# Kernel optimization log

Measured on AMD Instinct MI355X. Metric: run time of the kernel, lower is better.

Reference implementation:

```python
import jax, jax.numpy as jnp
import numpy as np

B, C, N = 4, 256, 4096
OUT = 256
TEMP = OUT ** 0.5  # temperature = sqrt(out_channel)


def setup_inputs() -> dict:
    key = jax.random.key(0)
    kx, kxx, kq, kk, kv = jax.random.split(key, 5)
    x = jax.random.normal(kx, (B, C, N), dtype=jnp.float32)
    xx = jax.random.normal(kxx, (B, C, N), dtype=jnp.float32)
    # Conv1d(in, out, kernel=1, bias=False) weights, squeezed to (out, in)
    s = 1.0 / np.sqrt(C)
    Wq = jax.random.uniform(kq, (OUT, C), jnp.float32, -s, s)
    Wk = jax.random.uniform(kk, (OUT, C), jnp.float32, -s, s)
    Wv = jax.random.uniform(kv, (OUT, C), jnp.float32, -s, s)
    return {"x": x, "xx": xx, "Wq": Wq, "Wk": Wk, "Wv": Wv}


def reference(x, xx, Wq, Wk, Wv):
    # 1x1 conv == per-point linear: (out,in) x (b,in,n) -> (b,out,n)
    q = jnp.einsum('oc,bcn->bon', Wq, x)
    k = jnp.einsum('oc,bcn->bon', Wk, xx)
    v = jnp.einsum('oc,bcn->bon', Wv, xx)
    # attn = (q^T / temp) @ k : (B, N, N)
    attn = jax.nn.softmax(jnp.einsum('bon,bom->bnm', q, k) / TEMP, axis=-1)
    # dropout is identity in eval mode
    # y = attn @ v^T -> (B, N, OUT); returned transposed to (B, OUT, N)
    y = jnp.einsum('bnm,bom->bon', attn, v)
    return y
```

## Files before the change

### kernel.cpp

```cpp
#include <hip/hip_runtime.h>
#include <hip/hip_bf16.h>


typedef __attribute__((ext_vector_type(8))) short bf16x8;
typedef __attribute__((ext_vector_type(4))) float f32x4;
typedef __attribute__((ext_vector_type(4))) short short4t;

constexpr int B_ = 4;
constexpr int C_ = 256;
constexpr int N_ = 4096;
constexpr int O_ = 256;
constexpr float INV_TEMP = 1.0f / 16.0f;
constexpr int NIT = 64;

__device__ __forceinline__ short f2bf(float f) {
  union { float f; unsigned u; } v; v.f = f;
  unsigned r = v.u + 0x7fffu + ((v.u >> 16) & 1u);
  return (short)(r >> 16);
}

__device__ __forceinline__ void dma16(const short* g, short* l) {
  __builtin_amdgcn_global_load_lds(
      (const __attribute__((address_space(1))) unsigned int*)g,
      (__attribute__((address_space(3))) unsigned int*)l, 16, 0, 0);
}

__global__ void wcvt(const float* __restrict__ Wq, const float* __restrict__ Wk,
                     const float* __restrict__ Wv, short* __restrict__ wb) {
  int i = blockIdx.x * 256 + threadIdx.x;
  int mat = i >> 16, off = i & 65535;
  const float* W = (mat == 0) ? Wq : (mat == 1 ? Wk : Wv);
  wb[i] = f2bf(W[off]);
}

__global__ __launch_bounds__(256, 2) void qkv_proj(
    const float* __restrict__ x, const float* __restrict__ xx,
    const short* __restrict__ wb,
    short* __restrict__ qg, short* __restrict__ kt, short* __restrict__ vt) {
  const int n0  = blockIdx.x * 64;
  const int b   = blockIdx.y;
  const int mat = blockIdx.z;
  const float* src = (mat == 0) ? x : xx;
  const short* W   = wb + mat * 65536;
  const int tid = threadIdx.x;
  const int w = tid >> 6, lane = tid & 63;
  const int g = lane >> 4, c16 = lane & 15;

  __shared__ __align__(16) short xs[64][264];

  {
    const int n = tid & 63, cq = tid >> 6;
    const float* sp = src + (size_t)b * C_ * N_ + n0 + n;
#pragma unroll
    for (int rep = 0; rep < 16; ++rep) {
      int c = rep * 16 + cq * 4;
      short4t s4;
#pragma unroll
      for (int j = 0; j < 4; ++j) s4[j] = f2bf(sp[(size_t)(c + j) * N_]);
      *(short4t*)&xs[n][c] = s4;
    }
  }
  __syncthreads();

  f32x4 acc[4][4];
#pragma unroll
  for (int i = 0; i < 4; ++i)
#pragma unroll
    for (int j = 0; j < 4; ++j) acc[i][j] = (f32x4){0.f, 0.f, 0.f, 0.f};

#pragma unroll
  for (int ko = 0; ko < 8; ++ko) {
    bf16x8 wfr[4], xfr[4];
#pragma unroll
    for (int ot = 0; ot < 4; ++ot)
      wfr[ot] = *(const bf16x8*)&W[(w * 64 + ot * 16 + c16) * C_ + ko * 32 + g * 8];
#pragma unroll
    for (int nt = 0; nt < 4; ++nt)
      xfr[nt] = *(const bf16x8*)&xs[nt * 16 + c16][ko * 32 + g * 8];
    if (mat < 2) {
#pragma unroll
      for (int ot = 0; ot < 4; ++ot)
#pragma unroll
        for (int nt = 0; nt < 4; ++nt)
          acc[ot][nt] = __builtin_amdgcn_mfma_f32_16x16x32_bf16(
              wfr[ot], xfr[nt], acc[ot][nt], 0, 0, 0);
    } else {
#pragma unroll
      for (int mt = 0; mt < 4; ++mt)
#pragma unroll
        for (int ot = 0; ot < 4; ++ot)
          acc[mt][ot] = __builtin_amdgcn_mfma_f32_16x16x32_bf16(
              xfr[mt], wfr[ot], acc[mt][ot], 0, 0, 0);
    }
  }

  __syncthreads();
  short* ob = &xs[0][0];

  if (mat == 0) {
#pragma unroll
    for (int ot = 0; ot < 4; ++ot)
#pragma unroll
      for (int nt = 0; nt < 4; ++nt) {
        int f = (nt * 16 + c16) * 256 + w * 64 + ot * 16 + g * 4;
        short4t s;
        s[0] = f2bf(acc[ot][nt][0] * INV_TEMP);
        s[1] = f2bf(acc[ot][nt][1] * INV_TEMP);
        s[2] = f2bf(acc[ot][nt][2] * INV_TEMP);
        s[3] = f2bf(acc[ot][nt][3] * INV_TEMP);
        *(short4t*)&ob[f] = s;
      }
  } else if (mat == 1) {
#pragma unroll
    for (int ot = 0; ot < 4; ++ot)
#pragma unroll
      for (int nt = 0; nt < 4; ++nt) {
        int koo = w * 2 + (ot >> 1);
        int pos = (((ot & 1) * 2 + (g >> 1)) ^ ((c16 >> 1) & 3));
        int f = nt * 4096 + koo * 512 + c16 * 32 + pos * 8 + (g & 1) * 4;
        short4t s;
        s[0] = f2bf(acc[ot][nt][0]);
        s[1] = f2bf(acc[ot][nt][1]);
        s[2] = f2bf(acc[ot][nt][2]);
        s[3] = f2bf(acc[ot][nt][3]);
        *(short4t*)&ob[f] = s;
      }
  } else {
#pragma unroll
    for (int mt = 0; mt < 4; ++mt)
#pragma unroll
      for (int ot = 0; ot < 4; ++ot) {
        int o = w * 64 + ot * 16 + c16;
        int pos = (mt * 2 + (g >> 1)) ^ (o & 7);
        int f = o * 64 + pos * 8 + (g & 1) * 4;
        short4t s;
        s[0] = f2bf(acc[mt][ot][0]);
        s[1] = f2bf(acc[mt][ot][1]);
        s[2] = f2bf(acc[mt][ot][2]);
        s[3] = f2bf(acc[mt][ot][3]);
        *(short4t*)&ob[f] = s;
      }
  }
  __syncthreads();

  short* dst = (mat == 0) ? qg + ((size_t)b * N_ + n0) * O_
             : (mat == 1) ? kt + (size_t)(b * 256 + (n0 >> 4)) * 4096
                          : vt + (size_t)(b * 64 + (n0 >> 6)) * 16384;
  const uint4* s4 = (const uint4*)ob;
  uint4* d4 = (uint4*)dst;
#pragma unroll
  for (int j = 0; j < 8; ++j) d4[j * 256 + tid] = s4[j * 256 + tid];
}

__global__ __launch_bounds__(512, 2) void flash_attn(
    const short* __restrict__ qg, const short* __restrict__ kt,
    const short* __restrict__ vt, float* __restrict__ out) {
  const int xg = blockIdx.x;
  const int b  = xg >> 1;
  const int n0 = (((xg & 1) << 5) + blockIdx.y) * 64;
  const int tid = threadIdx.x;
  const int w = tid >> 6, lane = tid & 63;
  const int g = lane >> 4, c16 = lane & 15;
  const bool prod = (w < 4);
  const int pw = w & 3;

  __shared__ short kb[2][16384];
  __shared__ short vb[2][16384];
  __shared__ short ps[2][64][72];
  __shared__ float lsum[4][64];

  const short* ktb = kt + (size_t)b * N_ * O_;
  const short* vtb = vt + (size_t)b * N_ * O_;

  bf16x8 qf[4][8];
  float lrun[4] = {0.f, 0.f, 0.f, 0.f};
  f32x4 oacc[4][4];
#pragma unroll
  for (int i = 0; i < 4; ++i)
#pragma unroll
    for (int j = 0; j < 4; ++j) oacc[i][j] = (f32x4){0.f, 0.f, 0.f, 0.f};

  if (prod) {
#pragma unroll
    for (int nt = 0; nt < 4; ++nt) {
      const short* qrow =
          qg + (size_t)(b * N_ + n0 + nt * 16 + c16) * O_ + g * 8;
#pragma unroll
      for (int ko = 0; ko < 8; ++ko)
        qf[nt][ko] = *(const bf16x8*)(qrow + ko * 32);
    }
    const short* src = ktb + (size_t)pw * 4096;
#pragma unroll
    for (int j = 0; j < 8; ++j)
      dma16(src + j * 512 + lane * 8, &kb[0][pw * 4096 + j * 512]);
  }
  __syncthreads();

  const int sw = (g ^ ((c16 >> 1) & 3)) * 8;

  for (int i = 0; i <= NIT; ++i) {
    if (prod) {
      if (i < NIT) {
        if (i + 1 < NIT) {
          const short* src = ktb + (size_t)(4 * (i + 1) + pw) * 4096;
          short* dst = &kb[(i + 1) & 1][pw * 4096];
#pragma unroll
          for (int j = 0; j < 8; ++j)
            dma16(src + j * 512 + lane * 8, dst + j * 512);
        }
        const short* ksl = &kb[i & 1][pw * 4096];
        f32x4 sacc[4];
#pragma unroll
        for (int nt = 0; nt < 4; ++nt) sacc[nt] = (f32x4){0.f, 0.f, 0.f, 0.f};
#pragma unroll
        for (int ko = 0; ko < 8; ++ko) {
          bf16x8 kf = *(const bf16x8*)&ksl[(ko * 16 + c16) * 32 + sw];
#pragma unroll
          for (int nt = 0; nt < 4; ++nt)
            sacc[nt] = __builtin_amdgcn_mfma_f32_16x16x32_bf16(
                kf, qf[nt][ko], sacc[nt], 0, 0, 0);
        }
#pragma unroll
        for (int nt = 0; nt < 4; ++nt) {
          short4t pb;
          float rs = 0.f;
#pragma unroll
          for (int r = 0; r < 4; ++r) {
            float p = __expf(sacc[nt][r]);
            rs += p;
            pb[r] = f2bf(p);
          }
          lrun[nt] += rs;
          *(short4t*)&ps[i & 1][nt * 16 + c16][pw * 16 + g * 4] = pb;
        }
      }
    } else {
      if (i < NIT) {
        const short* src = vtb + (size_t)i * 16384 + pw * 4096;
        short* dst = &vb[i & 1][pw * 4096];
#pragma unroll
        for (int j = 0; j < 8; ++j)
          dma16(src + j * 512 + lane * 8, dst + j * 512);
      }
      if (i > 0) {
        const int pb_ = (i - 1) & 1;
#pragma unroll
        for (int kk = 0; kk < 2; ++kk) {
          bf16x8 pf[4];
#pragma unroll
          for (int nt = 0; nt < 4; ++nt)
            pf[nt] = *(const bf16x8*)&ps[pb_][nt * 16 + c16][kk * 32 + g * 8];
#pragma unroll
          for (int ot = 0; ot < 4; ++ot) {
            int pos = (kk * 4 + g) ^ (c16 & 7);
            bf16x8 vf = *(const bf16x8*)
                &vb[pb_][(pw * 64 + ot * 16 + c16) * 64 + pos * 8];
#pragma unroll
            for (int nt = 0; nt < 4; ++nt)
              oacc[ot][nt] = __builtin_amdgcn_mfma_f32_16x16x32_bf16(
                  vf, pf[nt], oacc[ot][nt], 0, 0, 0);
          }
        }
      }
    }
    __syncthreads();
  }

  if (prod) {
#pragma unroll
    for (int nt = 0; nt < 4; ++nt) {
      float v = lrun[nt];
      v += __shfl_xor(v, 16);
      v += __shfl_xor(v, 32);
      if (lane < 16) lsum[pw][nt * 16 + lane] = v;
    }
  }
  __syncthreads();
  if (!prod) {
#pragma unroll
    for (int nt = 0; nt < 4; ++nt) {
      const int nl = nt * 16 + c16;
      float l = lsum[0][nl] + lsum[1][nl] + lsum[2][nl] + lsum[3][nl];
      float li = 1.0f / l;
#pragma unroll
      for (int ot = 0; ot < 4; ++ot) {
        float* op = out + ((size_t)b * O_ + pw * 64 + ot * 16 + g * 4) * N_ +
                    n0 + nl;
#pragma unroll
        for (int r = 0; r < 4; ++r)
          op[(size_t)r * N_] = oacc[ot][nt][r] * li;
      }
    }
  }
}

extern "C" void kernel_launch(void* const* d_in, const int* in_sizes, int n_in,
                              void* d_out, int out_size, void* d_ws,
                              size_t ws_size, hipStream_t stream) {
  const float* x  = (const float*)d_in[0];
  const float* xx = (const float*)d_in[1];
  const float* Wq = (const float*)d_in[2];
  const float* Wk = (const float*)d_in[3];
  const float* Wv = (const float*)d_in[4];
  float* out = (float*)d_out;

  short* qg = (short*)d_ws;
  short* kt = qg + (size_t)B_ * N_ * O_;
  short* vt = kt + (size_t)B_ * N_ * O_;
  short* wb = vt + (size_t)B_ * N_ * O_;

  wcvt<<<768, 256, 0, stream>>>(Wq, Wk, Wv, wb);
  qkv_proj<<<dim3(N_ / 64, B_, 3), 256, 0, stream>>>(x, xx, wb, qg, kt, vt);
  flash_attn<<<dim3(8, 32), 512, 0, stream>>>(qg, kt, vt, out);
}
```

Baseline: 207.3 us.

## Pre-transpose inputs to bf16 in a separate kernel and fold temperature into Wq

Adds an xpose kernel that DMAs fp32 x/xx tiles into LDS and writes them transposed as bf16 (N-major). It stages this scratch copy in the output buffer, which flash_attn later overwrites. qkv_proj then reads its MFMA operand fragments straight from global bf16 instead of doing strided fp32 loads and conversion into LDS. The 1/temperature scale moves into the Wq bf16 conversion, so the Q epilogue no longer multiplies. The cost is an extra launch and an extra write and read of the transposed inputs.

After: 217.0 us. 4.7% more time.

```diff
diff --git a/kernel.cpp b/kernel.cpp
--- a/kernel.cpp
+++ b/kernel.cpp
@@ -19,7 +19,7 @@
   return (short)(r >> 16);
 }
 
-__device__ __forceinline__ void dma16(const short* g, short* l) {
+__device__ __forceinline__ void dma16(const void* g, void* l) {
   __builtin_amdgcn_global_load_lds(
       (const __attribute__((address_space(1))) unsigned int*)g,
       (__attribute__((address_space(3))) unsigned int*)l, 16, 0, 0);
@@ -30,37 +30,58 @@
   int i = blockIdx.x * 256 + threadIdx.x;
   int mat = i >> 16, off = i & 65535;
   const float* W = (mat == 0) ? Wq : (mat == 1 ? Wk : Wv);
-  wb[i] = f2bf(W[off]);
+  float v = W[off];
+  if (mat == 0) v *= INV_TEMP;
+  wb[i] = f2bf(v);
+}
+
+__global__ __launch_bounds__(256, 2) void xpose(
+    const float* __restrict__ x, const float* __restrict__ xx,
+    short* __restrict__ xb) {
+  const int nt = blockIdx.x;
+  const int ct = blockIdx.y;
+  const int b  = blockIdx.z >> 1;
+  const int inp = blockIdx.z & 1;
+  const float* src = (inp ? xx : x) + (size_t)b * C_ * N_;
+  const int tid = threadIdx.x;
+  const int w = tid >> 6, lane = tid & 63;
+
+  __shared__ float tl[64][256];
+
+  {
+    const float* rp = src + (size_t)(ct * 64 + w * 16) * N_ + nt * 256 + lane * 4;
+#pragma unroll
+    for (int j = 0; j < 16; ++j)
+      dma16(rp + (size_t)j * N_, &tl[w * 16 + j][0]);
+  }
+  __syncthreads();
+
+  {
+    const int n = tid;
+    short* orow = xb + ((size_t)(inp * B_ + b) * N_ + nt * 256 + n) * C_ + ct * 64;
+#pragma unroll
+    for (int oct = 0; oct < 8; ++oct) {
+      bf16x8 v;
+#pragma unroll
+      for (int j = 0; j < 8; ++j) v[j] = f2bf(tl[oct * 8 + j][n]);
+      *(bf16x8*)(orow + oct * 8) = v;
+    }
+  }
 }
 
 __global__ __launch_bounds__(256, 2) void qkv_proj(
-    const float* __restrict__ x, const float* __restrict__ xx,
-    const short* __restrict__ wb,
+    const short* __restrict__ xb, const short* __restrict__ wb,
     short* __restrict__ qg, short* __restrict__ kt, short* __restrict__ vt) {
   const int n0  = blockIdx.x * 64;
   const int b   = blockIdx.y;
   const int mat = blockIdx.z;
-  const float* src = (mat == 0) ? x : xx;
+  const short* xbb = xb + (size_t)(((mat > 0) ? B_ : 0) + b) * N_ * C_;
   const short* W   = wb + mat * 65536;
   const int tid = threadIdx.x;
   const int w = tid >> 6, lane = tid & 63;
   const int g = lane >> 4, c16 = lane & 15;
 
-  __shared__ __align__(16) short xs[64][264];
-
-  {
-    const int n = tid & 63, cq = tid >> 6;
-    const float* sp = src + (size_t)b * C_ * N_ + n0 + n;
-#pragma unroll
-    for (int rep = 0; rep < 16; ++rep) {
-      int c = rep * 16 + cq * 4;
-      short4t s4;
-#pragma unroll
-      for (int j = 0; j < 4; ++j) s4[j] = f2bf(sp[(size_t)(c + j) * N_]);
-      *(short4t*)&xs[n][c] = s4;
-    }
-  }
-  __syncthreads();
+  __shared__ __align__(16) short obuf[16384];
 
   f32x4 acc[4][4];
 #pragma unroll
@@ -76,7 +97,8 @@
       wfr[ot] = *(const bf16x8*)&W[(w * 64 + ot * 16 + c16) * C_ + ko * 32 + g * 8];
 #pragma unroll
     for (int nt = 0; nt < 4; ++nt)
-      xfr[nt] = *(const bf16x8*)&xs[nt * 16 + c16][ko * 32 + g * 8];
+      xfr[nt] = *(const bf16x8*)
+          &xbb[(size_t)(n0 + nt * 16 + c16) * C_ + ko * 32 + g * 8];
     if (mat < 2) {
 #pragma unroll
       for (int ot = 0; ot < 4; ++ot)
@@ -94,9 +116,6 @@
     }
   }
 
-  __syncthreads();
-  short* ob = &xs[0][0];
-
   if (mat == 0) {
 #pragma unroll
     for (int ot = 0; ot < 4; ++ot)
@@ -104,11 +123,11 @@
       for (int nt = 0; nt < 4; ++nt) {
         int f = (nt * 16 + c16) * 256 + w * 64 + ot * 16 + g * 4;
         short4t s;
-        s[0] = f2bf(acc[ot][nt][0] * INV_TEMP);
-        s[1] = f2bf(acc[ot][nt][1] * INV_TEMP);
-        s[2] = f2bf(acc[ot][nt][2] * INV_TEMP);
-        s[3] = f2bf(acc[ot][nt][3] * INV_TEMP);
-        *(short4t*)&ob[f] = s;
+        s[0] = f2bf(acc[ot][nt][0]);
+        s[1] = f2bf(acc[ot][nt][1]);
+        s[2] = f2bf(acc[ot][nt][2]);
+        s[3] = f2bf(acc[ot][nt][3]);
+        *(short4t*)&obuf[f] = s;
       }
   } else if (mat == 1) {
 #pragma unroll
@@ -123,7 +142,7 @@
         s[1] = f2bf(acc[ot][nt][1]);
         s[2] = f2bf(acc[ot][nt][2]);
         s[3] = f2bf(acc[ot][nt][3]);
-        *(short4t*)&ob[f] = s;
+        *(short4t*)&obuf[f] = s;
       }
   } else {
 #pragma unroll
@@ -138,7 +157,7 @@
         s[1] = f2bf(acc[mt][ot][1]);
         s[2] = f2bf(acc[mt][ot][2]);
         s[3] = f2bf(acc[mt][ot][3]);
-        *(short4t*)&ob[f] = s;
+        *(short4t*)&obuf[f] = s;
       }
   }
   __syncthreads();
@@ -146,7 +165,7 @@
   short* dst = (mat == 0) ? qg + ((size_t)b * N_ + n0) * O_
              : (mat == 1) ? kt + (size_t)(b * 256 + (n0 >> 4)) * 4096
                           : vt + (size_t)(b * 64 + (n0 >> 6)) * 16384;
-  const uint4* s4 = (const uint4*)ob;
+  const uint4* s4 = (const uint4*)obuf;
   uint4* d4 = (uint4*)dst;
 #pragma unroll
   for (int j = 0; j < 8; ++j) d4[j * 256 + tid] = s4[j * 256 + tid];
@@ -303,6 +322,7 @@
   const float* Wk = (const float*)d_in[3];
   const float* Wv = (const float*)d_in[4];
   float* out = (float*)d_out;
+  short* xb = (short*)d_out;
 
   short* qg = (short*)d_ws;
   short* kt = qg + (size_t)B_ * N_ * O_;
@@ -310,6 +330,7 @@
   short* wb = vt + (size_t)B_ * N_ * O_;
 
   wcvt<<<768, 256, 0, stream>>>(Wq, Wk, Wv, wb);
-  qkv_proj<<<dim3(N_ / 64, B_, 3), 256, 0, stream>>>(x, xx, wb, qg, kt, vt);
+  xpose<<<dim3(16, 4, 8), 256, 0, stream>>>(x, xx, xb);
+  qkv_proj<<<dim3(N_ / 64, B_, 3), 256, 0, stream>>>(xb, wb, qg, kt, vt);
   flash_attn<<<dim3(8, 32), 512, 0, stream>>>(qg, kt, vt, out);
 }
```

## Double flash-attention waves per block and fold weight conversion into projection

Applied to the files above, without the earlier changes.

The flash attention block grows from 512 to 1024 threads. There are now 8 producer waves, each computing scores for half the query rows of a key slice, and 8 consumer waves, each owning 32 output channels instead of 64. This halves per-wave register state and MFMA work and aims to hide latency better with more waves per CU. The separate weight-conversion kernel is removed: qkv_proj now reads the fp32 weights directly, converts them to bf16 in-register and folds the 1/temp scale into Wq. That saves one launch, but every projection block repeats the weight conversion, and the launch-bounds hint of 4 blocks of 1024 threads may push register limits.

Result: slower. 229.4 us (+10.7%).

```diff
diff --git a/kernel.cpp b/kernel.cpp
--- a/kernel.cpp
+++ b/kernel.cpp
@@ -19,29 +19,23 @@
   return (short)(r >> 16);
 }
 
-__device__ __forceinline__ void dma16(const short* g, short* l) {
+__device__ __forceinline__ void dma16(const void* g, void* l) {
   __builtin_amdgcn_global_load_lds(
       (const __attribute__((address_space(1))) unsigned int*)g,
       (__attribute__((address_space(3))) unsigned int*)l, 16, 0, 0);
 }
 
-__global__ void wcvt(const float* __restrict__ Wq, const float* __restrict__ Wk,
-                     const float* __restrict__ Wv, short* __restrict__ wb) {
-  int i = blockIdx.x * 256 + threadIdx.x;
-  int mat = i >> 16, off = i & 65535;
-  const float* W = (mat == 0) ? Wq : (mat == 1 ? Wk : Wv);
-  wb[i] = f2bf(W[off]);
-}
-
 __global__ __launch_bounds__(256, 2) void qkv_proj(
     const float* __restrict__ x, const float* __restrict__ xx,
-    const short* __restrict__ wb,
+    const float* __restrict__ Wq, const float* __restrict__ Wk,
+    const float* __restrict__ Wv,
     short* __restrict__ qg, short* __restrict__ kt, short* __restrict__ vt) {
   const int n0  = blockIdx.x * 64;
   const int b   = blockIdx.y;
   const int mat = blockIdx.z;
   const float* src = (mat == 0) ? x : xx;
-  const short* W   = wb + mat * 65536;
+  const float* Wm  = (mat == 0) ? Wq : (mat == 1 ? Wk : Wv);
+  const float ws   = (mat == 0) ? INV_TEMP : 1.0f;
   const int tid = threadIdx.x;
   const int w = tid >> 6, lane = tid & 63;
   const int g = lane >> 4, c16 = lane & 15;
@@ -72,8 +66,18 @@
   for (int ko = 0; ko < 8; ++ko) {
     bf16x8 wfr[4], xfr[4];
 #pragma unroll
-    for (int ot = 0; ot < 4; ++ot)
-      wfr[ot] = *(const bf16x8*)&W[(w * 64 + ot * 16 + c16) * C_ + ko * 32 + g * 8];
+    for (int ot = 0; ot < 4; ++ot) {
+      const float* wp =
+          Wm + (size_t)(w * 64 + ot * 16 + c16) * C_ + ko * 32 + g * 8;
+      float4 f0 = *(const float4*)wp;
+      float4 f1 = *(const float4*)(wp + 4);
+      bf16x8 a;
+      a[0] = f2bf(f0.x * ws); a[1] = f2bf(f0.y * ws);
+      a[2] = f2bf(f0.z * ws); a[3] = f2bf(f0.w * ws);
+      a[4] = f2bf(f1.x * ws); a[5] = f2bf(f1.y * ws);
+      a[6] = f2bf(f1.z * ws); a[7] = f2bf(f1.w * ws);
+      wfr[ot] = a;
+    }
 #pragma unroll
     for (int nt = 0; nt < 4; ++nt)
       xfr[nt] = *(const bf16x8*)&xs[nt * 16 + c16][ko * 32 + g * 8];
@@ -104,10 +108,10 @@
       for (int nt = 0; nt < 4; ++nt) {
         int f = (nt * 16 + c16) * 256 + w * 64 + ot * 16 + g * 4;
         short4t s;
-        s[0] = f2bf(acc[ot][nt][0] * INV_TEMP);
-        s[1] = f2bf(acc[ot][nt][1] * INV_TEMP);
-        s[2] = f2bf(acc[ot][nt][2] * INV_TEMP);
-        s[3] = f2bf(acc[ot][nt][3] * INV_TEMP);
+        s[0] = f2bf(acc[ot][nt][0]);
+        s[1] = f2bf(acc[ot][nt][1]);
+        s[2] = f2bf(acc[ot][nt][2]);
+        s[3] = f2bf(acc[ot][nt][3]);
         *(short4t*)&ob[f] = s;
       }
   } else if (mat == 1) {
@@ -152,7 +156,7 @@
   for (int j = 0; j < 8; ++j) d4[j * 256 + tid] = s4[j * 256 + tid];
 }
 
-__global__ __launch_bounds__(512, 2) void flash_attn(
+__global__ __launch_bounds__(1024, 4) void flash_attn(
     const short* __restrict__ qg, const short* __restrict__ kt,
     const short* __restrict__ vt, float* __restrict__ out) {
   const int xg = blockIdx.x;
@@ -161,8 +165,10 @@
   const int tid = threadIdx.x;
   const int w = tid >> 6, lane = tid & 63;
   const int g = lane >> 4, c16 = lane & 15;
-  const bool prod = (w < 4);
-  const int pw = w & 3;
+  const bool prod = (w < 8);
+  const int ga = w & 3;
+  const int h  = (w >> 2) & 1;
+  const int cw = w & 7;
 
   __shared__ short kb[2][16384];
   __shared__ short vb[2][16384];
@@ -172,27 +178,28 @@
   const short* ktb = kt + (size_t)b * N_ * O_;
   const short* vtb = vt + (size_t)b * N_ * O_;
 
-  bf16x8 qf[4][8];
-  float lrun[4] = {0.f, 0.f, 0.f, 0.f};
-  f32x4 oacc[4][4];
-#pragma unroll
-  for (int i = 0; i < 4; ++i)
+  bf16x8 qf[2][8];
+  float lrun[2] = {0.f, 0.f};
+  f32x4 oacc[2][4];
+#pragma unroll
+  for (int i = 0; i < 2; ++i)
 #pragma unroll
     for (int j = 0; j < 4; ++j) oacc[i][j] = (f32x4){0.f, 0.f, 0.f, 0.f};
 
   if (prod) {
 #pragma unroll
-    for (int nt = 0; nt < 4; ++nt) {
+    for (int j = 0; j < 2; ++j) {
       const short* qrow =
-          qg + (size_t)(b * N_ + n0 + nt * 16 + c16) * O_ + g * 8;
+          qg + (size_t)(b * N_ + n0 + (h * 2 + j) * 16 + c16) * O_ + g * 8;
 #pragma unroll
       for (int ko = 0; ko < 8; ++ko)
-        qf[nt][ko] = *(const bf16x8*)(qrow + ko * 32);
-    }
-    const short* src = ktb + (size_t)pw * 4096;
-#pragma unroll
-    for (int j = 0; j < 8; ++j)
-      dma16(src + j * 512 + lane * 8, &kb[0][pw * 4096 + j * 512]);
+        qf[j][ko] = *(const bf16x8*)(qrow + ko * 32);
+    }
+    const short* src = ktb + (size_t)(w >> 1) * 4096 + (w & 1) * 2048;
+    short* dst = &kb[0][(w >> 1) * 4096 + (w & 1) * 2048];
+#pragma unroll
+    for (int j = 0; j < 4; ++j)
+      dma16(src + j * 512 + lane * 8, dst + j * 512);
   }
   __syncthreads();
 
@@ -202,44 +209,45 @@
     if (prod) {
       if (i < NIT) {
         if (i + 1 < NIT) {
-          const short* src = ktb + (size_t)(4 * (i + 1) + pw) * 4096;
-          short* dst = &kb[(i + 1) & 1][pw * 4096];
-#pragma unroll
-          for (int j = 0; j < 8; ++j)
+          const short* src =
+              ktb + (size_t)(4 * (i + 1) + (w >> 1)) * 4096 + (w & 1) * 2048;
+          short* dst = &kb[(i + 1) & 1][(w >> 1) * 4096 + (w & 1) * 2048];
+#pragma unroll
+          for (int j = 0; j < 4; ++j)
             dma16(src + j * 512 + lane * 8, dst + j * 512);
         }
-        const short* ksl = &kb[i & 1][pw * 4096];
-        f32x4 sacc[4];
-#pragma unroll
-        for (int nt = 0; nt < 4; ++nt) sacc[nt] = (f32x4){0.f, 0.f, 0.f, 0.f};
+        const short* ksl = &kb[i & 1][ga * 4096];
+        f32x4 sacc[2];
+        sacc[0] = (f32x4){0.f, 0.f, 0.f, 0.f};
+        sacc[1] = (f32x4){0.f, 0.f, 0.f, 0.f};
 #pragma unroll
         for (int ko = 0; ko < 8; ++ko) {
           bf16x8 kf = *(const bf16x8*)&ksl[(ko * 16 + c16) * 32 + sw];
 #pragma unroll
-          for (int nt = 0; nt < 4; ++nt)
-            sacc[nt] = __builtin_amdgcn_mfma_f32_16x16x32_bf16(
-                kf, qf[nt][ko], sacc[nt], 0, 0, 0);
+          for (int j = 0; j < 2; ++j)
+            sacc[j] = __builtin_amdgcn_mfma_f32_16x16x32_bf16(
+                kf, qf[j][ko], sacc[j], 0, 0, 0);
         }
 #pragma unroll
-        for (int nt = 0; nt < 4; ++nt) {
+        for (int j = 0; j < 2; ++j) {
           short4t pb;
           float rs = 0.f;
 #pragma unroll
           for (int r = 0; r < 4; ++r) {
-            float p = __expf(sacc[nt][r]);
+            float p = __expf(sacc[j][r]);
             rs += p;
             pb[r] = f2bf(p);
           }
-          lrun[nt] += rs;
-          *(short4t*)&ps[i & 1][nt * 16 + c16][pw * 16 + g * 4] = pb;
+          lrun[j] += rs;
+          *(short4t*)&ps[i & 1][(h * 2 + j) * 16 + c16][ga * 16 + g * 4] = pb;
         }
       }
     } else {
       if (i < NIT) {
-        const short* src = vtb + (size_t)i * 16384 + pw * 4096;
-        short* dst = &vb[i & 1][pw * 4096];
-#pragma unroll
-        for (int j = 0; j < 8; ++j)
+        const short* src = vtb + (size_t)i * 16384 + cw * 2048;
+        short* dst = &vb[i & 1][cw * 2048];
+#pragma unroll
+        for (int j = 0; j < 4; ++j)
           dma16(src + j * 512 + lane * 8, dst + j * 512);
       }
       if (i > 0) {
@@ -251,10 +259,10 @@
           for (int nt = 0; nt < 4; ++nt)
             pf[nt] = *(const bf16x8*)&ps[pb_][nt * 16 + c16][kk * 32 + g * 8];
 #pragma unroll
-          for (int ot = 0; ot < 4; ++ot) {
-            int pos = (kk * 4 + g) ^ (c16 & 7);
-            bf16x8 vf = *(const bf16x8*)
-                &vb[pb_][(pw * 64 + ot * 16 + c16) * 64 + pos * 8];
+          for (int ot = 0; ot < 2; ++ot) {
+            int o = cw * 32 + ot * 16 + c16;
+            int pos = (kk * 4 + g) ^ (o & 7);
+            bf16x8 vf = *(const bf16x8*)&vb[pb_][o * 64 + pos * 8];
 #pragma unroll
             for (int nt = 0; nt < 4; ++nt)
               oacc[ot][nt] = __builtin_amdgcn_mfma_f32_16x16x32_bf16(
@@ -268,11 +276,11 @@
 
   if (prod) {
 #pragma unroll
-    for (int nt = 0; nt < 4; ++nt) {
-      float v = lrun[nt];
+    for (int j = 0; j < 2; ++j) {
+      float v = lrun[j];
       v += __shfl_xor(v, 16);
       v += __shfl_xor(v, 32);
-      if (lane < 16) lsum[pw][nt * 16 + lane] = v;
+      if (lane < 16) lsum[ga][h * 32 + j * 16 + lane] = v;
     }
   }
   __syncthreads();
@@ -283,8 +291,8 @@
       float l = lsum[0][nl] + lsum[1][nl] + lsum[2][nl] + lsum[3][nl];
       float li = 1.0f / l;
 #pragma unroll
-      for (int ot = 0; ot < 4; ++ot) {
-        float* op = out + ((size_t)b * O_ + pw * 64 + ot * 16 + g * 4) * N_ +
+      for (int ot = 0; ot < 2; ++ot) {
+        float* op = out + ((size_t)b * O_ + cw * 32 + ot * 16 + g * 4) * N_ +
                     n0 + nl;
 #pragma unroll
         for (int r = 0; r < 4; ++r)
@@ -307,9 +315,8 @@
   short* qg = (short*)d_ws;
   short* kt = qg + (size_t)B_ * N_ * O_;
   short* vt = kt + (size_t)B_ * N_ * O_;
-  short* wb = vt + (size_t)B_ * N_ * O_;
-
-  wcvt<<<768, 256, 0, stream>>>(Wq, Wk, Wv, wb);
-  qkv_proj<<<dim3(N_ / 64, B_, 3), 256, 0, stream>>>(x, xx, wb, qg, kt, vt);
-  flash_attn<<<dim3(8, 32), 512, 0, stream>>>(qg, kt, vt, out);
-}
+
+  qkv_proj<<<dim3(N_ / 64, B_, 3), 256, 0, stream>>>(x, xx, Wq, Wk, Wv, qg,
+                                                     kt, vt);
+  flash_attn<<<dim3(8, 32), 1024, 0, stream>>>(qg, kt, vt, out);
+}
```

## Load V tiles straight to registers and fuse weight conversion into projection

Applied to the files above, without the earlier changes.

The attention kernel now prefetches V fragments directly from global memory into a double-buffered register array instead of DMA-staging them in shared memory. The main loop is unrolled by two so buffer indices are compile-time constants. The separate weight-conversion kernel is removed: the projection kernel converts fp32 weights to bf16 on the fly and folds the temperature scale into Wq. This cuts a launch and LDS traffic, but raises register pressure and repeats weight conversion in every block.

New measurement: 321.9 us. 55.3% more time.

```diff
diff --git a/kernel.cpp b/kernel.cpp
--- a/kernel.cpp
+++ b/kernel.cpp
@@ -19,29 +19,23 @@
   return (short)(r >> 16);
 }
 
-__device__ __forceinline__ void dma16(const short* g, short* l) {
+__device__ __forceinline__ void dma16(const void* g, void* l) {
   __builtin_amdgcn_global_load_lds(
       (const __attribute__((address_space(1))) unsigned int*)g,
       (__attribute__((address_space(3))) unsigned int*)l, 16, 0, 0);
 }
 
-__global__ void wcvt(const float* __restrict__ Wq, const float* __restrict__ Wk,
-                     const float* __restrict__ Wv, short* __restrict__ wb) {
-  int i = blockIdx.x * 256 + threadIdx.x;
-  int mat = i >> 16, off = i & 65535;
-  const float* W = (mat == 0) ? Wq : (mat == 1 ? Wk : Wv);
-  wb[i] = f2bf(W[off]);
-}
-
 __global__ __launch_bounds__(256, 2) void qkv_proj(
     const float* __restrict__ x, const float* __restrict__ xx,
-    const short* __restrict__ wb,
+    const float* __restrict__ Wq, const float* __restrict__ Wk,
+    const float* __restrict__ Wv,
     short* __restrict__ qg, short* __restrict__ kt, short* __restrict__ vt) {
   const int n0  = blockIdx.x * 64;
   const int b   = blockIdx.y;
   const int mat = blockIdx.z;
   const float* src = (mat == 0) ? x : xx;
-  const short* W   = wb + mat * 65536;
+  const float* Wm  = (mat == 0) ? Wq : (mat == 1 ? Wk : Wv);
+  const float ws   = (mat == 0) ? INV_TEMP : 1.0f;
   const int tid = threadIdx.x;
   const int w = tid >> 6, lane = tid & 63;
   const int g = lane >> 4, c16 = lane & 15;
@@ -72,8 +66,18 @@
   for (int ko = 0; ko < 8; ++ko) {
     bf16x8 wfr[4], xfr[4];
 #pragma unroll
-    for (int ot = 0; ot < 4; ++ot)
-      wfr[ot] = *(const bf16x8*)&W[(w * 64 + ot * 16 + c16) * C_ + ko * 32 + g * 8];
+    for (int ot = 0; ot < 4; ++ot) {
+      const float* wp =
+          Wm + (size_t)(w * 64 + ot * 16 + c16) * C_ + ko * 32 + g * 8;
+      float4 f0 = *(const float4*)wp;
+      float4 f1 = *(const float4*)(wp + 4);
+      bf16x8 a;
+      a[0] = f2bf(f0.x * ws); a[1] = f2bf(f0.y * ws);
+      a[2] = f2bf(f0.z * ws); a[3] = f2bf(f0.w * ws);
+      a[4] = f2bf(f1.x * ws); a[5] = f2bf(f1.y * ws);
+      a[6] = f2bf(f1.z * ws); a[7] = f2bf(f1.w * ws);
+      wfr[ot] = a;
+    }
 #pragma unroll
     for (int nt = 0; nt < 4; ++nt)
       xfr[nt] = *(const bf16x8*)&xs[nt * 16 + c16][ko * 32 + g * 8];
@@ -104,10 +108,10 @@
       for (int nt = 0; nt < 4; ++nt) {
         int f = (nt * 16 + c16) * 256 + w * 64 + ot * 16 + g * 4;
         short4t s;
-        s[0] = f2bf(acc[ot][nt][0] * INV_TEMP);
-        s[1] = f2bf(acc[ot][nt][1] * INV_TEMP);
-        s[2] = f2bf(acc[ot][nt][2] * INV_TEMP);
-        s[3] = f2bf(acc[ot][nt][3] * INV_TEMP);
+        s[0] = f2bf(acc[ot][nt][0]);
+        s[1] = f2bf(acc[ot][nt][1]);
+        s[2] = f2bf(acc[ot][nt][2]);
+        s[3] = f2bf(acc[ot][nt][3]);
         *(short4t*)&ob[f] = s;
       }
   } else if (mat == 1) {
@@ -152,6 +156,72 @@
   for (int j = 0; j < 8; ++j) d4[j * 256 + tid] = s4[j * 256 + tid];
 }
 
+#define PSTEP(I, CUR)                                                        \
+  if (prod) {                                                                \
+    if ((I) < NIT) {                                                         \
+      if ((I) + 1 < NIT) {                   \
+        const short* src = ktb + (size_t)(4 * ((I) + 1) + pw) * 4096;        \
+        short* dst = &kb[(CUR) ^ 1][pw * 4096];                              \
+        _Pragma("unroll")                                                    \
+        for (int j = 0; j < 8; ++j)                                          \
+          dma16(src + j * 512 + lane * 8, dst + j * 512);                    \
+      }                                                                      \
+      const short* ksl = &kb[(CUR)][pw * 4096];                              \
+      f32x4 sacc[4];                                                         \
+      _Pragma("unroll")                                                      \
+      for (int nt = 0; nt < 4; ++nt) sacc[nt] = (f32x4){0.f, 0.f, 0.f, 0.f};\
+      _Pragma("unroll")                                                      \
+      for (int ko = 0; ko < 8; ++ko) {                                       \
+        bf16x8 kf = *(const bf16x8*)&ksl[(ko * 16 + c16) * 32 + sw];         \
+        _Pragma("unroll")                                                    \
+        for (int nt = 0; nt < 4; ++nt)                                       \
+          sacc[nt] = __builtin_amdgcn_mfma_f32_16x16x32_bf16(                \
+              kf, qf[nt][ko], sacc[nt], 0, 0, 0);                            \
+      }                                                                      \
+      _Pragma("unroll")                                                      \
+      for (int nt = 0; nt < 4; ++nt) {                                       \
+        short4t pb;                                                          \
+        float rs = 0.f;                                                      \
+        _Pragma("unroll")                                                    \
+        for (int r = 0; r < 4; ++r) {                                        \
+          float p = __expf(sacc[nt][r]);                                     \
+          rs += p;                                                           \
+          pb[r] = f2bf(p);                                                   \
+        }                                                                    \
+        lrun[nt] += rs;                                                      \
+        *(short4t*)&ps[(CUR)][nt * 16 + c16][pw * 16 + g * 4] = pb;          \
+      }                                                                      \
+    }                                                                        \
+  } else {                                                                   \
+    if ((I) < NIT) {          \
+      const short* vsrc = vtb + (size_t)(I) * 16384 + pw * 4096;             \
+      _Pragma("unroll")                                                      \
+      for (int ot = 0; ot < 4; ++ot)                                         \
+        _Pragma("unroll")                                                    \
+        for (int kk = 0; kk < 2; ++kk)                                       \
+          vreg[(CUR)][ot * 2 + kk] = *(const bf16x8*)                        \
+              &vsrc[(ot * 16 + c16) * 64 + (((kk * 4 + g) ^ (c16 & 7)) * 8)];\
+    }                                                                        \
+    if ((I) > 0) {                  \
+      _Pragma("unroll")                                                      \
+      for (int kk = 0; kk < 2; ++kk) {                                       \
+        bf16x8 pf[4];                                                        \
+        _Pragma("unroll")                                                    \
+        for (int nt = 0; nt < 4; ++nt)                                       \
+          pf[nt] = *(const bf16x8*)                                          \
+              &ps[(CUR) ^ 1][nt * 16 + c16][kk * 32 + g * 8];                \
+        _Pragma("unroll")                                                    \
+        for (int ot = 0; ot < 4; ++ot) {                                     \
+          bf16x8 vf = vreg[(CUR) ^ 1][ot * 2 + kk];                          \
+          _Pragma("unroll")                                                  \
+          for (int nt = 0; nt < 4; ++nt)                                     \
+            oacc[ot][nt] = __builtin_amdgcn_mfma_f32_16x16x32_bf16(          \
+                vf, pf[nt], oacc[ot][nt], 0, 0, 0);                          \
+        }                                                                    \
+      }                                                                      \
+    }                                                                        \
+  }
+
 __global__ __launch_bounds__(512, 2) void flash_attn(
     const short* __restrict__ qg, const short* __restrict__ kt,
     const short* __restrict__ vt, float* __restrict__ out) {
@@ -165,7 +235,6 @@
   const int pw = w & 3;
 
   __shared__ short kb[2][16384];
-  __shared__ short vb[2][16384];
   __shared__ short ps[2][64][72];
   __shared__ float lsum[4][64];
 
@@ -173,6 +242,7 @@
   const short* vtb = vt + (size_t)b * N_ * O_;
 
   bf16x8 qf[4][8];
+  bf16x8 vreg[2][8];
   float lrun[4] = {0.f, 0.f, 0.f, 0.f};
   f32x4 oacc[4][4];
 #pragma unroll
@@ -198,73 +268,14 @@
 
   const int sw = (g ^ ((c16 >> 1) & 3)) * 8;
 
-  for (int i = 0; i <= NIT; ++i) {
-    if (prod) {
-      if (i < NIT) {
-        if (i + 1 < NIT) {
-          const short* src = ktb + (size_t)(4 * (i + 1) + pw) * 4096;
-          short* dst = &kb[(i + 1) & 1][pw * 4096];
-#pragma unroll
-          for (int j = 0; j < 8; ++j)
-            dma16(src + j * 512 + lane * 8, dst + j * 512);
-        }
-        const short* ksl = &kb[i & 1][pw * 4096];
-        f32x4 sacc[4];
-#pragma unroll
-        for (int nt = 0; nt < 4; ++nt) sacc[nt] = (f32x4){0.f, 0.f, 0.f, 0.f};
-#pragma unroll
-        for (int ko = 0; ko < 8; ++ko) {
-          bf16x8 kf = *(const bf16x8*)&ksl[(ko * 16 + c16) * 32 + sw];
-#pragma unroll
-          for (int nt = 0; nt < 4; ++nt)
-            sacc[nt] = __builtin_amdgcn_mfma_f32_16x16x32_bf16(
-                kf, qf[nt][ko], sacc[nt], 0, 0, 0);
-        }
-#pragma unroll
-        for (int nt = 0; nt < 4; ++nt) {
-          short4t pb;
-          float rs = 0.f;
-#pragma unroll
-          for (int r = 0; r < 4; ++r) {
-            float p = __expf(sacc[nt][r]);
-            rs += p;
-            pb[r] = f2bf(p);
-          }
-          lrun[nt] += rs;
-          *(short4t*)&ps[i & 1][nt * 16 + c16][pw * 16 + g * 4] = pb;
-        }
-      }
-    } else {
-      if (i < NIT) {
-        const short* src = vtb + (size_t)i * 16384 + pw * 4096;
-        short* dst = &vb[i & 1][pw * 4096];
-#pragma unroll
-        for (int j = 0; j < 8; ++j)
-          dma16(src + j * 512 + lane * 8, dst + j * 512);
-      }
-      if (i > 0) {
-        const int pb_ = (i - 1) & 1;
-#pragma unroll
-        for (int kk = 0; kk < 2; ++kk) {
-          bf16x8 pf[4];
-#pragma unroll
-          for (int nt = 0; nt < 4; ++nt)
-            pf[nt] = *(const bf16x8*)&ps[pb_][nt * 16 + c16][kk * 32 + g * 8];
-#pragma unroll
-          for (int ot = 0; ot < 4; ++ot) {
-            int pos = (kk * 4 + g) ^ (c16 & 7);
-            bf16x8 vf = *(const bf16x8*)
-                &vb[pb_][(pw * 64 + ot * 16 + c16) * 64 + pos * 8];
-#pragma unroll
-            for (int nt = 0; nt < 4; ++nt)
-              oacc[ot][nt] = __builtin_amdgcn_mfma_f32_16x16x32_bf16(
-                  vf, pf[nt], oacc[ot][nt], 0, 0, 0);
-          }
-        }
-      }
-    }
+  for (int ih = 0; ih < NIT / 2; ++ih) {
+    PSTEP(2 * ih, 0);
     __syncthreads();
-  }
+    PSTEP(2 * ih + 1, 1);
+    __syncthreads();
+  }
+  PSTEP(NIT, 0);
+  __syncthreads();
 
   if (prod) {
 #pragma unroll
@@ -307,9 +318,8 @@
   short* qg = (short*)d_ws;
   short* kt = qg + (size_t)B_ * N_ * O_;
   short* vt = kt + (size_t)B_ * N_ * O_;
-  short* wb = vt + (size_t)B_ * N_ * O_;
-
-  wcvt<<<768, 256, 0, stream>>>(Wq, Wk, Wv, wb);
-  qkv_proj<<<dim3(N_ / 64, B_, 3), 256, 0, stream>>>(x, xx, wb, qg, kt, vt);
+
+  qkv_proj<<<dim3(N_ / 64, B_, 3), 256, 0, stream>>>(x, xx, Wq, Wk, Wv, qg,
+                                                     kt, vt);
   flash_attn<<<dim3(8, 32), 512, 0, stream>>>(qg, kt, vt, out);
 }
```
